# Kernel tuning notes

Measured on AMD Instinct MI355X. Metric: run time of the kernel, lower is better.

## Reference

```python
import jax, jax.numpy as jnp
import numpy as np

H, N, LMAX, KCH = 128, 64, 256, 2  # d_model, d_state, l_max per axis, kernel channels (bidirectional)


def _ssm_kernel(A_re, A_im, C_re, C_im, log_dt, L):
    """S4D diagonal SSM kernel (ZOH discretization) -> real kernel (KCH, H, L)."""
    A = A_re + 1j * A_im                      # (H, N)
    C = C_re + 1j * C_im                      # (KCH, H, N)
    dt = jnp.exp(log_dt)                      # (H,)
    dtA = dt[:, None] * A                     # (H, N)
    K = C * (jnp.exp(dtA) - 1.0) / A          # (KCH, H, N)
    vand = jnp.exp(dtA[:, :, None] * jnp.arange(L, dtype=dtA.real.dtype))  # (H, N, L)
    return 2.0 * jnp.einsum('chn,hnl->chl', K, vand).real


def _bidir_pad(k, L_in):
    """Split 2 kernel channels into fwd/bwd, flip backward one, pad to length Lk+L_in."""
    k0, k1 = k[:1], k[1:]                     # each (1, H, Lk)
    fwd = jnp.pad(k0, ((0, 0), (0, 0), (0, L_in)))
    bwd = jnp.pad(k1[..., ::-1], ((0, 0), (0, 0), (L_in, 0)))
    return fwd + bwd                          # (1, H, Lk + L_in)


def setup_inputs() -> dict:
    key = jax.random.key(0)
    ks = jax.random.split(key, 8)
    B, L1, L2 = 2, 256, 256
    u = jax.random.normal(ks[0], (B, H, L1, L2), jnp.float32)
    D = jax.random.normal(ks[1], (1, H), jnp.float32)

    def kparams(k_c, k_ci, k_dt):
        A_re = -0.5 * jnp.ones((H, N), jnp.float32)
        A_im = jnp.pi * jnp.broadcast_to(jnp.arange(N, dtype=jnp.float32), (H, N))
        C_re = jax.random.normal(k_c, (KCH, H, N), jnp.float32) * (0.5 ** 0.5)
        C_im = jax.random.normal(k_ci, (KCH, H, N), jnp.float32) * (0.5 ** 0.5)
        log_dt = jax.random.uniform(k_dt, (H,), jnp.float32,
                                    minval=np.log(1e-3), maxval=np.log(1e-1))
        return A_re, A_im, C_re, C_im, log_dt

    A_re0, A_im0, C_re0, C_im0, log_dt0 = kparams(ks[2], ks[3], ks[4])
    A_re1, A_im1, C_re1, C_im1, log_dt1 = kparams(ks[5], ks[6], ks[7])
    return {"u": u, "D": D,
            "A_re0": A_re0, "A_im0": A_im0, "C_re0": C_re0, "C_im0": C_im0, "log_dt0": log_dt0,
            "A_re1": A_re1, "A_im1": A_im1, "C_re1": C_re1, "C_im1": C_im1, "log_dt1": log_dt1}


def reference(u, D, A_re0, A_im0, C_re0, C_im0, log_dt0,
              A_re1, A_im1, C_re1, C_im1, log_dt1):
    B, _, L1, L2 = u.shape
    Lk1, Lk2 = min(L1, LMAX), min(L2, LMAX)
    # per-axis SSM kernels, then bidirectional flip-and-pad
    k1 = _bidir_pad(_ssm_kernel(A_re0, A_im0, C_re0, C_im0, log_dt0, Lk1), L1)  # (1,H,P1)
    k2 = _bidir_pad(_ssm_kernel(A_re1, A_im1, C_re1, C_im1, log_dt1, Lk2), L2)  # (1,H,P2)
    P1, P2 = L1 + Lk1, L2 + Lk2
    # N-D FFT convolution
    u_f = jnp.fft.rfftn(u, s=(P1, P2), axes=(-2, -1))        # (B,H,P1,P2//2+1)
    kf1 = jnp.fft.fft(k1, n=P1, axis=-1)                     # (1,H,P1) complex
    kf2 = jnp.fft.rfft(k2, n=P2, axis=-1)                    # (1,H,P2//2+1)
    k_f = jnp.einsum('chm,chn->chmn', kf1, kf2)              # outer product over axes (trank=1)
    y_f = jnp.einsum('bhmn,chmn->bchmn', u_f, k_f)           # (B,1,H,P1,P2r)
    y = jnp.fft.irfftn(y_f, s=(P1, P2), axes=(-2, -1))[..., :L1, :L2]
    # skip connection D
    y = y + jnp.einsum('bhxy,ch->bchxy', u, D)
    return y.reshape(B, -1, L1, L2)                          # (B, C*H, L1, L2)
```

## Files before the change

### kernel.cpp

```cpp
#include <hip/hip_runtime.h>

#define HH 128
#define NN 64
#define LL 256
#define WP 280

typedef __attribute__((ext_vector_type(8))) short bf8;
typedef __attribute__((ext_vector_type(4))) float f32x4;

__device__ inline ushort f2bf(float f) {
    uint x = __float_as_uint(f);
    return (ushort)((x + 0x7fffu + ((x >> 16) & 1u)) >> 16);
}
__device__ inline uint cvt_pk_bf16(float lo, float hi) {
    uint r;
    asm volatile("v_cvt_pk_bf16_f32 %0, %1, %2" : "=v"(r) : "v"(lo), "v"(hi));
    return r;
}
#define MFMA(a,b,c) __builtin_amdgcn_mfma_f32_16x16x32_bf16((a),(b),(c),0,0,0)

__global__ __launch_bounds__(512) void ssm_gen_fast(
    const float* __restrict__ A_re0, const float* __restrict__ A_im0,
    const float* __restrict__ C_re0, const float* __restrict__ C_im0,
    const float* __restrict__ log_dt0,
    const float* __restrict__ A_re1, const float* __restrict__ A_im1,
    const float* __restrict__ C_re1, const float* __restrict__ C_im1,
    const float* __restrict__ log_dt1,
    uint* __restrict__ arrg)
{
    __shared__ float4 par[128];
    __shared__ float  red[512];
    __shared__ ushort rev[512];

    int tid = threadIdx.x;
    int h   = blockIdx.x;
    int s   = blockIdx.y;

    if (tid < 128) {
        int n  = tid & 63;
        int ch = tid >> 6;
        const float* Ar = s ? A_re1 : A_re0;
        const float* Ai = s ? A_im1 : A_im0;
        const float* Cr = s ? C_re1 : C_re0;
        const float* Ci = s ? C_im1 : C_im0;
        const float* Ld = s ? log_dt1 : log_dt0;
        float dt = __expf(Ld[h]);
        float ar = Ar[h*NN + n], ai = Ai[h*NN + n];
        float cr = Cr[(ch*HH + h)*NN + n], ci = Ci[(ch*HH + h)*NN + n];
        float xr = dt * ar, xi = dt * ai;
        float phr = xi * 0.15915494f;
        float phf = phr - floorf(phr);
        float sn = __sinf(6.2831853f * phf);
        float cs = __cosf(6.2831853f * phf);
        float e  = __expf(xr);
        float er = e*cs - 1.f, ei = e*sn;
        float inv = 1.f / (ar*ar + ai*ai);
        float dr = (er*ar + ei*ai) * inv;
        float di = (ei*ar - er*ai) * inv;
        float Kr = 2.f*(cr*dr - ci*di);
        float Ki = 2.f*(cr*di + ci*dr);
        par[tid] = (float4){ xr, xi * 0.15915494f, Kr, Ki };
    }
    __syncthreads();

    {
        int l  = tid & 255;
        int ch = tid >> 8;
        float lf = (float)l;
#pragma unroll
        for (int nh = 0; nh < 2; ++nh) {
            const float4* pb = &par[ch*64 + nh*32];
            float acc = 0.f;
            for (int n = 0; n < 32; ++n) {
                float4 p = pb[n];
                float mag = __expf(p.x * lf);
                float ph  = p.y * lf;
                float phf = ph - floorf(ph);
                float ang = 6.2831853f * phf;
                acc += p.z * (mag * __cosf(ang)) - p.w * (mag * __sinf(ang));
            }
            if (nh == 0) red[tid] = acc;
            else {
                int ri = ch ? (256 + l) : (255 - l);
                rev[ri] = f2bf(red[tid] + acc);
            }
        }
    }
    __syncthreads();

    {
        int j  = tid & 255;
        uint lo, hi;
        if (tid < 256) { lo = rev[2*j];     hi = rev[2*j + 1]; }
        else           { lo = rev[2*j + 1]; hi = (j == 255) ? 0u : (uint)rev[2*j + 2]; }
        arrg[(s*HH + h)*512 + tid] = lo | (hi << 16);
    }
}

__global__ __launch_bounds__(512, 4) void s4nd_v4(
    const float* __restrict__ u, const float* __restrict__ Dv,
    const uint* __restrict__ arrg, float* __restrict__ out)
{
    __shared__ ushort WT[128 * WP];
    __shared__ uint   arr[2][512];

    int tid = threadIdx.x;

    int j    = blockIdx.x;
    int xcd  = j & 7;
    int k    = j >> 3;
    int bh   = xcd * 32 + (k >> 1);
    int y0   = (k & 1) * 128;
    int h    = bh & (HH - 1);

    arr[0][tid] = arrg[h*512 + tid];
    arr[1][tid] = arrg[(HH + h)*512 + tid];
    __syncthreads();

    int lane = tid & 63;
    int w = tid >> 6;
    int c = lane & 15, q = lane >> 4;
    int wm2 = (w >> 1) * 64, wn2 = (w & 1) * 64;

    const uint* T1 = &arr[0][(c & 1) ? 0 : 256];
    const uint* T2 = &arr[1][(c & 1) ? 0 : 256];
    int jb2 = (255 - y0  - c + 8*q) >> 1;
    int jb1 = (255 - wm2 - c + 8*q) >> 1;

    f32x4 acc[16];
#pragma unroll
    for (int i = 0; i < 16; ++i) acc[i] = (f32x4){0.f,0.f,0.f,0.f};

    const float* ub = u + (size_t)bh * LL * LL;
    const float* rp0 = ub + (size_t)(w*32 +  0 + c) * LL;
    const float* rp1 = ub + (size_t)(w*32 + 16 + c) * LL;

    bf8 win[8];
#pragma unroll
    for (int t = -7; t <= 0; ++t) {
        int jj = jb2 + 8*t;
        uint* pw = (uint*)&win[t & 7];
        pw[0] = T2[jj]; pw[1] = T2[jj+1]; pw[2] = T2[jj+2]; pw[3] = T2[jj+3];
    }
#pragma unroll
    for (int kk = 0; kk < 8; ++kk) {
        if (kk) {
#pragma unroll
            for (int t = 2*kk - 1; t <= 2*kk; ++t) {
                int jj = jb2 + 8*t;
                uint* pw = (uint*)&win[t & 7];
                pw[0] = T2[jj]; pw[1] = T2[jj+1]; pw[2] = T2[jj+2]; pw[3] = T2[jj+3];
            }
        }
        int yb = kk*32 + 8*q;
        float4 A0 = *(const float4*)(rp0 + yb);
        float4 A1 = *(const float4*)(rp0 + yb + 4);
        float4 A2 = *(const float4*)(rp1 + yb);
        float4 A3 = *(const float4*)(rp1 + yb + 4);
        bf8 b0, b1;
        uint* p0 = (uint*)&b0; uint* p1 = (uint*)&b1;
        p0[0] = cvt_pk_bf16(A0.x, A0.y); p0[1] = cvt_pk_bf16(A0.z, A0.w);
        p0[2] = cvt_pk_bf16(A1.x, A1.y); p0[3] = cvt_pk_bf16(A1.z, A1.w);
        p1[0] = cvt_pk_bf16(A2.x, A2.y); p1[1] = cvt_pk_bf16(A2.z, A2.w);
        p1[2] = cvt_pk_bf16(A3.x, A3.y); p1[3] = cvt_pk_bf16(A3.z, A3.w);
        __builtin_amdgcn_s_setprio(1);
#pragma unroll
        for (int mi = 0; mi < 8; ++mi) {
            bf8 a = win[(2*kk - mi) & 7];
            acc[mi*2 + 0] = MFMA(a, b0, acc[mi*2 + 0]);
            acc[mi*2 + 1] = MFMA(a, b1, acc[mi*2 + 1]);
        }
        __builtin_amdgcn_s_setprio(0);
    }

#pragma unroll
    for (int mi = 0; mi < 8; ++mi)
#pragma unroll
        for (int ni = 0; ni < 2; ++ni)
#pragma unroll
            for (int r = 0; r < 4; ++r) {
                int row = 16*mi + 4*q + r;
                int col = w*32 + 16*ni + c;
                WT[row*WP + col] = f2bf(acc[mi*2 + ni][r]);
                acc[mi*2 + ni][r] = 0.f;
            }
    __syncthreads();

    bf8 win2[4];
#pragma unroll
    for (int t = -3; t <= 0; ++t) {
        int jj = jb1 + 8*t;
        uint* pw = (uint*)&win2[t & 3];
        pw[0] = T1[jj]; pw[1] = T1[jj+1]; pw[2] = T1[jj+2]; pw[3] = T1[jj+3];
    }
#pragma unroll
    for (int kk = 0; kk < 8; ++kk) {
        if (kk) {
#pragma unroll
            for (int t = 2*kk - 1; t <= 2*kk; ++t) {
                int jj = jb1 + 8*t;
                uint* pw = (uint*)&win2[t & 3];
                pw[0] = T1[jj]; pw[1] = T1[jj+1]; pw[2] = T1[jj+2]; pw[3] = T1[jj+3];
            }
        }
        int xb = kk*32;
        bf8 b[4];
#pragma unroll
        for (int ni = 0; ni < 4; ++ni)
            b[ni] = *(const bf8*)&WT[(wn2 + 16*ni + c)*WP + xb + 8*q];
        __builtin_amdgcn_s_setprio(1);
#pragma unroll
        for (int mi = 0; mi < 4; ++mi) {
            bf8 a = win2[(2*kk - mi) & 3];
#pragma unroll
            for (int ni = 0; ni < 4; ++ni)
                acc[mi*4 + ni] = MFMA(a, b[ni], acc[mi*4 + ni]);
        }
        __builtin_amdgcn_s_setprio(0);
    }

    float dh = Dv[h];
    float* yb_ = out + (size_t)bh * LL * LL;
#pragma unroll
    for (int mi = 0; mi < 4; ++mi)
#pragma unroll
        for (int ni = 0; ni < 4; ++ni)
#pragma unroll
            for (int r = 0; r < 4; ++r) {
                int row = wm2 + 16*mi + 4*q + r;
                int col = y0 + wn2 + 16*ni + c;
                size_t o = (size_t)row * LL + col;
                yb_[o] = acc[mi*4 + ni][r] + dh * ub[o];
            }
}

extern "C" void kernel_launch(void* const* d_in, const int* in_sizes, int n_in,
                              void* d_out, int out_size, void* d_ws, size_t ws_size,
                              hipStream_t stream)
{
    const float* u       = (const float*)d_in[0];
    const float* D       = (const float*)d_in[1];
    const float* A_re0   = (const float*)d_in[2];
    const float* A_im0   = (const float*)d_in[3];
    const float* C_re0   = (const float*)d_in[4];
    const float* C_im0   = (const float*)d_in[5];
    const float* log_dt0 = (const float*)d_in[6];
    const float* A_re1   = (const float*)d_in[7];
    const float* A_im1   = (const float*)d_in[8];
    const float* C_re1   = (const float*)d_in[9];
    const float* C_im1   = (const float*)d_in[10];
    const float* log_dt1 = (const float*)d_in[11];
    float* out = (float*)d_out;

    uint* arrg = (uint*)d_ws;

    ssm_gen_fast<<<dim3(HH, 2), 512, 0, stream>>>(
        A_re0, A_im0, C_re0, C_im0, log_dt0,
        A_re1, A_im1, C_re1, C_im1, log_dt1, arrg);
    s4nd_v4<<<512, 512, 0, stream>>>(u, D, arrg, out);
}
```

Baseline: 49.45 us.

## Warp-specialized producer/consumer pipeline over column quarters, one block per (b,h)

Replaces the two-blocks-per-(b,h) design, where each block recomputed the full first-axis convolution for its half of the columns, with one block per (b,h). Two warp groups alternate: one runs the first-axis convolution for a 64-column quarter into a double-buffered shared tile while the other consumes the previous quarter with the second-axis convolution and writes the output. This removes the duplicated first-stage work and overlaps the two stages. In exchange the grid halves to 256 blocks, there are five barrier-separated steps with half the waves idle in the first and last, and occupancy is lowered to 2 blocks per CU.

```diff
diff --git a/kernel.cpp b/kernel.cpp
--- a/kernel.cpp
+++ b/kernel.cpp
@@ -97,141 +97,165 @@
     }
 }
 
-__global__ __launch_bounds__(512, 4) void s4nd_v4(
+__global__ __launch_bounds__(512, 2) void s4nd_ws(
     const float* __restrict__ u, const float* __restrict__ Dv,
     const uint* __restrict__ arrg, float* __restrict__ out)
 {
-    __shared__ ushort WT[128 * WP];
+    __shared__ ushort WT0[64 * WP];
+    __shared__ ushort WT1[64 * WP];
     __shared__ uint   arr[2][512];
 
     int tid = threadIdx.x;
-
-    int j    = blockIdx.x;
-    int xcd  = j & 7;
-    int k    = j >> 3;
-    int bh   = xcd * 32 + (k >> 1);
-    int y0   = (k & 1) * 128;
-    int h    = bh & (HH - 1);
+    int j   = blockIdx.x;
+    int bh  = (j & 7) * 32 + (j >> 3);
+    int h   = bh & (HH - 1);
 
     arr[0][tid] = arrg[h*512 + tid];
     arr[1][tid] = arrg[(HH + h)*512 + tid];
     __syncthreads();
 
     int lane = tid & 63;
-    int w = tid >> 6;
-    int c = lane & 15, q = lane >> 4;
-    int wm2 = (w >> 1) * 64, wn2 = (w & 1) * 64;
+    int w    = tid >> 6;
+    int c    = lane & 15, q = lane >> 4;
+    int grp  = w >> 2;
+    int sub  = w & 3;
 
     const uint* T1 = &arr[0][(c & 1) ? 0 : 256];
     const uint* T2 = &arr[1][(c & 1) ? 0 : 256];
-    int jb2 = (255 - y0  - c + 8*q) >> 1;
-    int jb1 = (255 - wm2 - c + 8*q) >> 1;
+
+    const float* ub = u + (size_t)bh * LL * LL;
+    float* yb_ = out + (size_t)bh * LL * LL;
+    float dh = Dv[h];
+
+    const float* rp[4];
+#pragma unroll
+    for (int ni = 0; ni < 4; ++ni)
+        rp[ni] = ub + (size_t)(sub*64 + 16*ni + c) * LL;
+
+    int jbC = (255 - 64*sub - c + 8*q) >> 1;
 
     f32x4 acc[16];
 #pragma unroll
     for (int i = 0; i < 16; ++i) acc[i] = (f32x4){0.f,0.f,0.f,0.f};
 
-    const float* ub = u + (size_t)bh * LL * LL;
-    const float* rp0 = ub + (size_t)(w*32 +  0 + c) * LL;
-    const float* rp1 = ub + (size_t)(w*32 + 16 + c) * LL;
-
-    bf8 win[8];
-#pragma unroll
-    for (int t = -7; t <= 0; ++t) {
-        int jj = jb2 + 8*t;
-        uint* pw = (uint*)&win[t & 7];
-        pw[0] = T2[jj]; pw[1] = T2[jj+1]; pw[2] = T2[jj+2]; pw[3] = T2[jj+3];
-    }
-#pragma unroll
-    for (int kk = 0; kk < 8; ++kk) {
-        if (kk) {
-#pragma unroll
-            for (int t = 2*kk - 1; t <= 2*kk; ++t) {
-                int jj = jb2 + 8*t;
-                uint* pw = (uint*)&win[t & 7];
+    for (int s = 0; s < 5; ++s) {
+        bool isProd = (s < 4) && ((s & 1) == grp);
+        bool isCons = (s >= 1) && (((s - 1) & 1) == grp);
+
+        if (isProd) {
+            int qt = s;
+            int yq = qt * 64;
+            ushort* wtb = (qt & 1) ? WT1 : WT0;
+            int jb = (255 - yq - c + 8*q) >> 1;
+            bf8 win[4];
+#pragma unroll
+            for (int t = -3; t <= 0; ++t) {
+                int jj = jb + 8*t;
+                uint* pw = (uint*)&win[t & 3];
                 pw[0] = T2[jj]; pw[1] = T2[jj+1]; pw[2] = T2[jj+2]; pw[3] = T2[jj+3];
             }
-        }
-        int yb = kk*32 + 8*q;
-        float4 A0 = *(const float4*)(rp0 + yb);
-        float4 A1 = *(const float4*)(rp0 + yb + 4);
-        float4 A2 = *(const float4*)(rp1 + yb);
-        float4 A3 = *(const float4*)(rp1 + yb + 4);
-        bf8 b0, b1;
-        uint* p0 = (uint*)&b0; uint* p1 = (uint*)&b1;
-        p0[0] = cvt_pk_bf16(A0.x, A0.y); p0[1] = cvt_pk_bf16(A0.z, A0.w);
-        p0[2] = cvt_pk_bf16(A1.x, A1.y); p0[3] = cvt_pk_bf16(A1.z, A1.w);
-        p1[0] = cvt_pk_bf16(A2.x, A2.y); p1[1] = cvt_pk_bf16(A2.z, A2.w);
-        p1[2] = cvt_pk_bf16(A3.x, A3.y); p1[3] = cvt_pk_bf16(A3.z, A3.w);
-        __builtin_amdgcn_s_setprio(1);
-#pragma unroll
-        for (int mi = 0; mi < 8; ++mi) {
-            bf8 a = win[(2*kk - mi) & 7];
-            acc[mi*2 + 0] = MFMA(a, b0, acc[mi*2 + 0]);
-            acc[mi*2 + 1] = MFMA(a, b1, acc[mi*2 + 1]);
-        }
-        __builtin_amdgcn_s_setprio(0);
-    }
-
-#pragma unroll
-    for (int mi = 0; mi < 8; ++mi)
-#pragma unroll
-        for (int ni = 0; ni < 2; ++ni)
-#pragma unroll
-            for (int r = 0; r < 4; ++r) {
-                int row = 16*mi + 4*q + r;
-                int col = w*32 + 16*ni + c;
-                WT[row*WP + col] = f2bf(acc[mi*2 + ni][r]);
-                acc[mi*2 + ni][r] = 0.f;
-            }
-    __syncthreads();
-
-    bf8 win2[4];
-#pragma unroll
-    for (int t = -3; t <= 0; ++t) {
-        int jj = jb1 + 8*t;
-        uint* pw = (uint*)&win2[t & 3];
-        pw[0] = T1[jj]; pw[1] = T1[jj+1]; pw[2] = T1[jj+2]; pw[3] = T1[jj+3];
-    }
-#pragma unroll
-    for (int kk = 0; kk < 8; ++kk) {
-        if (kk) {
-#pragma unroll
-            for (int t = 2*kk - 1; t <= 2*kk; ++t) {
-                int jj = jb1 + 8*t;
+#pragma unroll
+            for (int kk = 0; kk < 8; ++kk) {
+                if (kk) {
+#pragma unroll
+                    for (int t = 2*kk - 1; t <= 2*kk; ++t) {
+                        int jj = jb + 8*t;
+                        uint* pw = (uint*)&win[t & 3];
+                        pw[0] = T2[jj]; pw[1] = T2[jj+1]; pw[2] = T2[jj+2]; pw[3] = T2[jj+3];
+                    }
+                }
+                int yb = kk*32 + 8*q;
+                bf8 b[4];
+#pragma unroll
+                for (int ni = 0; ni < 4; ++ni) {
+                    float4 fa = *(const float4*)(rp[ni] + yb);
+                    float4 fb = *(const float4*)(rp[ni] + yb + 4);
+                    uint* pb = (uint*)&b[ni];
+                    pb[0] = cvt_pk_bf16(fa.x, fa.y); pb[1] = cvt_pk_bf16(fa.z, fa.w);
+                    pb[2] = cvt_pk_bf16(fb.x, fb.y); pb[3] = cvt_pk_bf16(fb.z, fb.w);
+                }
+                __builtin_amdgcn_s_setprio(1);
+#pragma unroll
+                for (int mi = 0; mi < 4; ++mi) {
+                    bf8 a = win[(2*kk - mi) & 3];
+#pragma unroll
+                    for (int ni = 0; ni < 4; ++ni)
+                        acc[mi*4 + ni] = MFMA(a, b[ni], acc[mi*4 + ni]);
+                }
+                __builtin_amdgcn_s_setprio(0);
+            }
+#pragma unroll
+            for (int mi = 0; mi < 4; ++mi)
+#pragma unroll
+                for (int ni = 0; ni < 4; ++ni)
+#pragma unroll
+                    for (int r = 0; r < 4; ++r) {
+                        int row = 16*mi + 4*q + r;
+                        int col = sub*64 + 16*ni + c;
+                        wtb[row*WP + col] = f2bf(acc[mi*4 + ni][r]);
+                        acc[mi*4 + ni][r] = 0.f;
+                    }
+        } else if (isCons) {
+            int qt = s - 1;
+            int yq = qt * 64;
+            const ushort* wtb = (qt & 1) ? WT1 : WT0;
+            bf8 win2[4];
+#pragma unroll
+            for (int t = -3; t <= 0; ++t) {
+                int jj = jbC + 8*t;
                 uint* pw = (uint*)&win2[t & 3];
                 pw[0] = T1[jj]; pw[1] = T1[jj+1]; pw[2] = T1[jj+2]; pw[3] = T1[jj+3];
             }
+#pragma unroll
+            for (int kk = 0; kk < 8; ++kk) {
+                if (kk) {
+#pragma unroll
+                    for (int t = 2*kk - 1; t <= 2*kk; ++t) {
+                        int jj = jbC + 8*t;
+                        uint* pw = (uint*)&win2[t & 3];
+                        pw[0] = T1[jj]; pw[1] = T1[jj+1]; pw[2] = T1[jj+2]; pw[3] = T1[jj+3];
+                    }
+                }
+                int xb = kk*32 + 8*q;
+                bf8 b[4];
+#pragma unroll
+                for (int ni = 0; ni < 4; ++ni)
+                    b[ni] = *(const bf8*)&wtb[(16*ni + c)*WP + xb];
+                __builtin_amdgcn_s_setprio(1);
+#pragma unroll
+                for (int mi = 0; mi < 4; ++mi) {
+                    bf8 a = win2[(2*kk - mi) & 3];
+#pragma unroll
+                    for (int ni = 0; ni < 4; ++ni)
+                        acc[mi*4 + ni] = MFMA(a, b[ni], acc[mi*4 + ni]);
+                }
+                __builtin_amdgcn_s_setprio(0);
+            }
+#pragma unroll
+            for (int mi = 0; mi < 4; ++mi) {
+                float uh[16];
+#pragma unroll
+                for (int ni = 0; ni < 4; ++ni)
+#pragma unroll
+                    for (int r = 0; r < 4; ++r) {
+                        int row = 64*sub + 16*mi + 4*q + r;
+                        int col = yq + 16*ni + c;
+                        uh[ni*4 + r] = ub[(size_t)row*LL + col];
+                    }
+#pragma unroll
+                for (int ni = 0; ni < 4; ++ni)
+#pragma unroll
+                    for (int r = 0; r < 4; ++r) {
+                        int row = 64*sub + 16*mi + 4*q + r;
+                        int col = yq + 16*ni + c;
+                        yb_[(size_t)row*LL + col] =
+                            acc[mi*4 + ni][r] + dh * uh[ni*4 + r];
+                        acc[mi*4 + ni][r] = 0.f;
+                    }
+            }
         }
-        int xb = kk*32;
-        bf8 b[4];
-#pragma unroll
-        for (int ni = 0; ni < 4; ++ni)
-            b[ni] = *(const bf8*)&WT[(wn2 + 16*ni + c)*WP + xb + 8*q];
-        __builtin_amdgcn_s_setprio(1);
-#pragma unroll
-        for (int mi = 0; mi < 4; ++mi) {
-            bf8 a = win2[(2*kk - mi) & 3];
-#pragma unroll
-            for (int ni = 0; ni < 4; ++ni)
-                acc[mi*4 + ni] = MFMA(a, b[ni], acc[mi*4 + ni]);
-        }
-        __builtin_amdgcn_s_setprio(0);
-    }
-
-    float dh = Dv[h];
-    float* yb_ = out + (size_t)bh * LL * LL;
-#pragma unroll
-    for (int mi = 0; mi < 4; ++mi)
-#pragma unroll
-        for (int ni = 0; ni < 4; ++ni)
-#pragma unroll
-            for (int r = 0; r < 4; ++r) {
-                int row = wm2 + 16*mi + 4*q + r;
-                int col = y0 + wn2 + 16*ni + c;
-                size_t o = (size_t)row * LL + col;
-                yb_[o] = acc[mi*4 + ni][r] + dh * ub[o];
-            }
+        __syncthreads();
+    }
 }
 
 extern "C" void kernel_launch(void* const* d_in, const int* in_sizes, int n_in,
@@ -257,5 +281,5 @@
     ssm_gen_fast<<<dim3(HH, 2), 512, 0, stream>>>(
         A_re0, A_im0, C_re0, C_im0, log_dt0,
         A_re1, A_im1, C_re1, C_im1, log_dt1, arrg);
-    s4nd_v4<<<512, 512, 0, stream>>>(u, D, arrg, out);
-}
+    s4nd_ws<<<256, 512, 0, stream>>>(u, D, arrg, out);
+}
```

Result: slower. 76.60 us (+54.9%).

## Software-pipeline u loads with inline asm and split accumulators into halves

Applied to the files above, without the earlier changes.

Phase 1 now processes the two 16-row column strips one after another, so it needs only 8 accumulators instead of 16. It double-buffers the global loads of u using inline asm and explicit vmcnt waits, so the next k-step's data is in flight while the current MFMAs run. Phase 2 also works in two 32-column halves, prefetches the residual u values before its MFMA loop, and writes the output with nontemporal stores. The intent is to lower register pressure and hide global-load latency, at the cost of fragile hand-scheduled asm and more window reloads.

```diff
diff --git a/kernel.cpp b/kernel.cpp
--- a/kernel.cpp
+++ b/kernel.cpp
@@ -97,7 +97,46 @@
     }
 }
 
-__global__ __launch_bounds__(512, 4) void s4nd_v4(
+#define GL0(dst, addr)  asm volatile("global_load_dwordx4 %0, %1, off"           : "=v"(dst) : "v"(addr))
+#define GL16(dst, addr) asm volatile("global_load_dwordx4 %0, %1, off offset:16" : "=v"(dst) : "v"(addr))
+#define VMW(n) do { asm volatile("s_waitcnt vmcnt(" #n ")" ::: "memory"); \
+                    __builtin_amdgcn_sched_barrier(0); } while (0)
+
+#define WINROLL8(T, JB, t_)                                                   \
+    { int jj = (JB) + 8*(t_); uint* pw = (uint*)&win[(t_) & 7];               \
+      pw[0]=T[jj]; pw[1]=T[jj+1]; pw[2]=T[jj+2]; pw[3]=T[jj+3]; }
+
+#define PH1_KK(kk, C0, C1, N0, N1)                                            \
+    {                                                                         \
+        { const float* a_ = rp + ((kk)+1)*32 + 8*q;                           \
+          GL0(N0, a_); GL16(N1, a_); }                                        \
+        if ((kk) > 0) { WINROLL8(T2, jb2, 2*(kk)-1); WINROLL8(T2, jb2, 2*(kk)); } \
+        VMW(2);                                                               \
+        bf8 b0_; uint* pb_ = (uint*)&b0_;                                     \
+        pb_[0]=cvt_pk_bf16(C0.x,C0.y); pb_[1]=cvt_pk_bf16(C0.z,C0.w);         \
+        pb_[2]=cvt_pk_bf16(C1.x,C1.y); pb_[3]=cvt_pk_bf16(C1.z,C1.w);         \
+        __builtin_amdgcn_s_setprio(1);                                        \
+        _Pragma("unroll")                                                     \
+        for (int mi = 0; mi < 8; ++mi)                                        \
+            acc[mi] = MFMA(win[(2*(kk)-mi) & 7], b0_, acc[mi]);               \
+        __builtin_amdgcn_s_setprio(0);                                        \
+    }
+
+#define PH1_KK7(C0, C1)                                                       \
+    {                                                                         \
+        WINROLL8(T2, jb2, 13); WINROLL8(T2, jb2, 14);                         \
+        VMW(0);                                                               \
+        bf8 b0_; uint* pb_ = (uint*)&b0_;                                     \
+        pb_[0]=cvt_pk_bf16(C0.x,C0.y); pb_[1]=cvt_pk_bf16(C0.z,C0.w);         \
+        pb_[2]=cvt_pk_bf16(C1.x,C1.y); pb_[3]=cvt_pk_bf16(C1.z,C1.w);         \
+        __builtin_amdgcn_s_setprio(1);                                        \
+        _Pragma("unroll")                                                     \
+        for (int mi = 0; mi < 8; ++mi)                                        \
+            acc[mi] = MFMA(win[(14-mi) & 7], b0_, acc[mi]);                   \
+        __builtin_amdgcn_s_setprio(0);                                        \
+    }
+
+__global__ __launch_bounds__(512, 4) void s4nd_v5(
     const float* __restrict__ u, const float* __restrict__ Dv,
     const uint* __restrict__ arrg, float* __restrict__ out)
 {
@@ -105,7 +144,6 @@
     __shared__ uint   arr[2][512];
 
     int tid = threadIdx.x;
-
     int j    = blockIdx.x;
     int xcd  = j & 7;
     int k    = j >> 3;
@@ -127,111 +165,99 @@
     int jb2 = (255 - y0  - c + 8*q) >> 1;
     int jb1 = (255 - wm2 - c + 8*q) >> 1;
 
-    f32x4 acc[16];
-#pragma unroll
-    for (int i = 0; i < 16; ++i) acc[i] = (f32x4){0.f,0.f,0.f,0.f};
+    f32x4 acc[8];
+#pragma unroll
+    for (int i = 0; i < 8; ++i) acc[i] = (f32x4){0.f,0.f,0.f,0.f};
 
     const float* ub = u + (size_t)bh * LL * LL;
-    const float* rp0 = ub + (size_t)(w*32 +  0 + c) * LL;
-    const float* rp1 = ub + (size_t)(w*32 + 16 + c) * LL;
-
-    bf8 win[8];
-#pragma unroll
-    for (int t = -7; t <= 0; ++t) {
-        int jj = jb2 + 8*t;
-        uint* pw = (uint*)&win[t & 7];
-        pw[0] = T2[jj]; pw[1] = T2[jj+1]; pw[2] = T2[jj+2]; pw[3] = T2[jj+3];
-    }
-#pragma unroll
-    for (int kk = 0; kk < 8; ++kk) {
-        if (kk) {
-#pragma unroll
-            for (int t = 2*kk - 1; t <= 2*kk; ++t) {
-                int jj = jb2 + 8*t;
-                uint* pw = (uint*)&win[t & 7];
-                pw[0] = T2[jj]; pw[1] = T2[jj+1]; pw[2] = T2[jj+2]; pw[3] = T2[jj+3];
-            }
-        }
-        int yb = kk*32 + 8*q;
-        float4 A0 = *(const float4*)(rp0 + yb);
-        float4 A1 = *(const float4*)(rp0 + yb + 4);
-        float4 A2 = *(const float4*)(rp1 + yb);
-        float4 A3 = *(const float4*)(rp1 + yb + 4);
-        bf8 b0, b1;
-        uint* p0 = (uint*)&b0; uint* p1 = (uint*)&b1;
-        p0[0] = cvt_pk_bf16(A0.x, A0.y); p0[1] = cvt_pk_bf16(A0.z, A0.w);
-        p0[2] = cvt_pk_bf16(A1.x, A1.y); p0[3] = cvt_pk_bf16(A1.z, A1.w);
-        p1[0] = cvt_pk_bf16(A2.x, A2.y); p1[1] = cvt_pk_bf16(A2.z, A2.w);
-        p1[2] = cvt_pk_bf16(A3.x, A3.y); p1[3] = cvt_pk_bf16(A3.z, A3.w);
-        __builtin_amdgcn_s_setprio(1);
-#pragma unroll
-        for (int mi = 0; mi < 8; ++mi) {
-            bf8 a = win[(2*kk - mi) & 7];
-            acc[mi*2 + 0] = MFMA(a, b0, acc[mi*2 + 0]);
-            acc[mi*2 + 1] = MFMA(a, b1, acc[mi*2 + 1]);
-        }
-        __builtin_amdgcn_s_setprio(0);
-    }
-
-#pragma unroll
-    for (int mi = 0; mi < 8; ++mi)
-#pragma unroll
-        for (int ni = 0; ni < 2; ++ni)
+    float* yb_ = out + (size_t)bh * LL * LL;
+
+#pragma unroll
+    for (int ns = 0; ns < 2; ++ns) {
+        const float* rp = ub + (size_t)(w*32 + 16*ns + c) * LL;
+        bf8 win[8];
+#pragma unroll
+        for (int t = -7; t <= 0; ++t) WINROLL8(T2, jb2, t);
+        float4 SA0, SA1, SB0, SB1;
+        { const float* a_ = rp + 8*q; GL0(SA0, a_); GL16(SA1, a_); }
+        PH1_KK(0, SA0, SA1, SB0, SB1)
+        PH1_KK(1, SB0, SB1, SA0, SA1)
+        PH1_KK(2, SA0, SA1, SB0, SB1)
+        PH1_KK(3, SB0, SB1, SA0, SA1)
+        PH1_KK(4, SA0, SA1, SB0, SB1)
+        PH1_KK(5, SB0, SB1, SA0, SA1)
+        PH1_KK(6, SA0, SA1, SB0, SB1)
+        PH1_KK7(SB0, SB1)
+#pragma unroll
+        for (int mi = 0; mi < 8; ++mi)
 #pragma unroll
             for (int r = 0; r < 4; ++r) {
                 int row = 16*mi + 4*q + r;
-                int col = w*32 + 16*ni + c;
-                WT[row*WP + col] = f2bf(acc[mi*2 + ni][r]);
-                acc[mi*2 + ni][r] = 0.f;
-            }
-    __syncthreads();
-
-    bf8 win2[4];
-#pragma unroll
-    for (int t = -3; t <= 0; ++t) {
-        int jj = jb1 + 8*t;
-        uint* pw = (uint*)&win2[t & 3];
-        pw[0] = T1[jj]; pw[1] = T1[jj+1]; pw[2] = T1[jj+2]; pw[3] = T1[jj+3];
-    }
-#pragma unroll
-    for (int kk = 0; kk < 8; ++kk) {
-        if (kk) {
-#pragma unroll
-            for (int t = 2*kk - 1; t <= 2*kk; ++t) {
-                int jj = jb1 + 8*t;
-                uint* pw = (uint*)&win2[t & 3];
-                pw[0] = T1[jj]; pw[1] = T1[jj+1]; pw[2] = T1[jj+2]; pw[3] = T1[jj+3];
-            }
-        }
-        int xb = kk*32;
-        bf8 b[4];
-#pragma unroll
-        for (int ni = 0; ni < 4; ++ni)
-            b[ni] = *(const bf8*)&WT[(wn2 + 16*ni + c)*WP + xb + 8*q];
-        __builtin_amdgcn_s_setprio(1);
-#pragma unroll
-        for (int mi = 0; mi < 4; ++mi) {
-            bf8 a = win2[(2*kk - mi) & 3];
-#pragma unroll
-            for (int ni = 0; ni < 4; ++ni)
-                acc[mi*4 + ni] = MFMA(a, b[ni], acc[mi*4 + ni]);
-        }
-        __builtin_amdgcn_s_setprio(0);
-    }
+                WT[row*WP + w*32 + 16*ns + c] = f2bf(acc[mi][r]);
+                acc[mi][r] = 0.f;
+            }
+    }
+    __syncthreads();
 
     float dh = Dv[h];
-    float* yb_ = out + (size_t)bh * LL * LL;
-#pragma unroll
-    for (int mi = 0; mi < 4; ++mi)
-#pragma unroll
-        for (int ni = 0; ni < 4; ++ni)
+#pragma unroll
+    for (int p = 0; p < 2; ++p) {
+        int nb = wn2 + p*32;
+
+        float uh[32];
+#pragma unroll
+        for (int mi = 0; mi < 4; ++mi)
 #pragma unroll
             for (int r = 0; r < 4; ++r) {
                 int row = wm2 + 16*mi + 4*q + r;
-                int col = y0 + wn2 + 16*ni + c;
-                size_t o = (size_t)row * LL + col;
-                yb_[o] = acc[mi*4 + ni][r] + dh * ub[o];
-            }
+#pragma unroll
+                for (int ni = 0; ni < 2; ++ni)
+                    uh[(mi*4 + r)*2 + ni] = ub[(size_t)row*LL + y0 + nb + 16*ni + c];
+            }
+
+        bf8 win2[4];
+#pragma unroll
+        for (int t = -3; t <= 0; ++t) {
+            int jj = jb1 + 8*t;
+            uint* pw = (uint*)&win2[t & 3];
+            pw[0]=T1[jj]; pw[1]=T1[jj+1]; pw[2]=T1[jj+2]; pw[3]=T1[jj+3];
+        }
+#pragma unroll
+        for (int kk = 0; kk < 8; ++kk) {
+            if (kk) {
+#pragma unroll
+                for (int t = 2*kk - 1; t <= 2*kk; ++t) {
+                    int jj = jb1 + 8*t;
+                    uint* pw = (uint*)&win2[t & 3];
+                    pw[0]=T1[jj]; pw[1]=T1[jj+1]; pw[2]=T1[jj+2]; pw[3]=T1[jj+3];
+                }
+            }
+            int xb = kk*32 + 8*q;
+            bf8 b0 = *(const bf8*)&WT[(nb + c)*WP + xb];
+            bf8 b1 = *(const bf8*)&WT[(nb + 16 + c)*WP + xb];
+            __builtin_amdgcn_s_setprio(1);
+#pragma unroll
+            for (int mi = 0; mi < 4; ++mi) {
+                bf8 a = win2[(2*kk - mi) & 3];
+                acc[mi*2 + 0] = MFMA(a, b0, acc[mi*2 + 0]);
+                acc[mi*2 + 1] = MFMA(a, b1, acc[mi*2 + 1]);
+            }
+            __builtin_amdgcn_s_setprio(0);
+        }
+
+#pragma unroll
+        for (int mi = 0; mi < 4; ++mi)
+#pragma unroll
+            for (int ni = 0; ni < 2; ++ni)
+#pragma unroll
+                for (int r = 0; r < 4; ++r) {
+                    int row = wm2 + 16*mi + 4*q + r;
+                    int col = y0 + nb + 16*ni + c;
+                    float v = acc[mi*2 + ni][r] + dh * uh[(mi*4 + r)*2 + ni];
+                    __builtin_nontemporal_store(v, &yb_[(size_t)row*LL + col]);
+                    acc[mi*2 + ni][r] = 0.f;
+                }
+    }
 }
 
 extern "C" void kernel_launch(void* const* d_in, const int* in_sizes, int n_in,
@@ -257,5 +283,5 @@
     ssm_gen_fast<<<dim3(HH, 2), 512, 0, stream>>>(
         A_re0, A_im0, C_re0, C_im0, log_dt0,
         A_re1, A_im1, C_re1, C_im1, log_dt1, arrg);
-    s4nd_v4<<<512, 512, 0, stream>>>(u, D, arrg, out);
-}
+    s4nd_v5<<<512, 512, 0, stream>>>(u, D, arrg, out);
+}
```

After: 53.29 us. +7.8%, slower.
